# Performance work log

Hardware: AMD Instinct MI355X
Metric: run time of the kernel (lower is better)

The kernel has to match this reference:

```python
import jax, jax.numpy as jnp
import numpy as np

V = 6          # num_variables
K = 6          # codebook_size
D = 32         # embedding_dim
C = 3          # channels
B = 64         # batch
N = K ** V     # 46656 codebook combinations
EPS = 1e-5     # torch BatchNorm eps
ENTROPY_SCALE = 0.1


def setup_inputs() -> dict:
    key = jax.random.key(0)
    ks = jax.random.split(key, 40)
    i = iter(range(40))
    def rn(shape, s):
        return jax.random.normal(ks[next(i)], shape, dtype=jnp.float32) * s
    def rv(shape):
        return 0.5 + 0.5 * jax.random.uniform(ks[next(i)], shape, dtype=jnp.float32)
    inp = {
        'x': jax.random.normal(ks[next(i)], (B, C, 7, 7), dtype=jnp.float32),
        # encoder
        'conv_w': rn((256, C, 7, 7), 0.08), 'conv_b': rn((256,), 0.01),
        'ebn2_g': 1.0 + rn((256,), 0.1), 'ebn2_b': rn((256,), 0.1),
        'fc1_w': rn((1024, 256), 0.06), 'fc1_b': rn((1024,), 0.01),
        'ebn1_g': 1.0 + rn((1024,), 0.1), 'ebn1_b': rn((1024,), 0.1),
        'fc2_w': rn((V * K, 1024), 0.03), 'fc2_b': rn((V * K,), 0.01),
        # quantizer embeddings (V separate codebooks)
        'embeds': jax.random.normal(ks[next(i)], (V, K, D), dtype=jnp.float32),
        # decoder
        'dfc1_w': rn((1024, V * D), 0.07), 'dfc1_b': rn((1024,), 0.01),
        'dbn1_g': 1.0 + rn((1024,), 0.1), 'dbn1_b': rn((1024,), 0.1),
        'dbn1_rm': rn((1024,), 0.1), 'dbn1_rv': rv((1024,)),
        'dfc2_w': rn((256, 1024), 0.03), 'dfc2_b': rn((256,), 0.01),
        'dbn2_g': 1.0 + rn((256,), 0.1), 'dbn2_b': rn((256,), 0.1),
        'dbn2_rm': rn((256,), 0.1), 'dbn2_rv': rv((256,)),
        'dct1_w': rn((256, 16, 7, 7), 0.05), 'dct1_b': rn((16,), 0.01),
        'dbn3_g': 1.0 + rn((16,), 0.1), 'dbn3_b': rn((16,), 0.1),
        'dbn3_rm': rn((16,), 0.1), 'dbn3_rv': rv((16,)),
        'dct2_w': rn((16, C), 0.2), 'dct2_b': rn((C,), 0.01),
    }
    return inp


def _bn_eval(t, g, b, rm, rvar):
    # eval-mode BatchNorm (running stats); params broadcast over leading dims
    return g * (t - rm) * jax.lax.rsqrt(rvar + EPS) + b


def _bn_train(t, g, b):
    # train-mode BatchNorm1d on (B, F): biased batch statistics over dim 0
    m = t.mean(0)
    v = ((t - m) ** 2).mean(0)
    return g * (t - m) * jax.lax.rsqrt(v + EPS) + b


def _decode_all(embeds, dfc1_w, dfc1_b, dbn1_g, dbn1_b, dbn1_rm, dbn1_rv,
                dfc2_w, dfc2_b, dbn2_g, dbn2_b, dbn2_rm, dbn2_rv,
                dct1_w, dct1_b, dbn3_g, dbn3_b, dbn3_rm, dbn3_rv,
                dct2_w, dct2_b):
    # enumerate all K^V index tuples in itertools.product order (first var slowest)
    idx = jnp.arange(N)
    powers = K ** (V - 1 - jnp.arange(V))
    combos = (idx[:, None] // powers[None, :]) % K          # (N, V)
    z = embeds[jnp.arange(V)[None, :], combos]              # (N, V, D) gather
    h = z.reshape(N, V * D) @ dfc1_w.T + dfc1_b             # (N, 1024)
    h = jax.nn.relu(_bn_eval(h, dbn1_g, dbn1_b, dbn1_rm, dbn1_rv))
    h = h @ dfc2_w.T + dfc2_b                               # (N, 256)
    h = jax.nn.relu(_bn_eval(h, dbn2_g, dbn2_b, dbn2_rm, dbn2_rv))
    # ConvTranspose2d(256,16,7,stride=2) on 1x1 input == einsum with full kernel
    h = jnp.einsum('ni,iohw->nohw', h, dct1_w) + dct1_b[:, None, None]  # (N,16,7,7)
    h = jax.nn.relu(_bn_eval(h, dbn3_g[:, None, None], dbn3_b[:, None, None],
                             dbn3_rm[:, None, None], dbn3_rv[:, None, None]))
    # ConvTranspose2d(16,C,1,1) == pointwise channel mix
    em = jnp.einsum('nihw,io->nohw', h, dct2_w) + dct2_b[:, None, None]  # (N,C,7,7)
    return em


def reference(x, conv_w, conv_b, ebn2_g, ebn2_b, fc1_w, fc1_b, ebn1_g, ebn1_b,
              fc2_w, fc2_b, embeds, dfc1_w, dfc1_b, dbn1_g, dbn1_b, dbn1_rm,
              dbn1_rv, dfc2_w, dfc2_b, dbn2_g, dbn2_b, dbn2_rm, dbn2_rv,
              dct1_w, dct1_b, dbn3_g, dbn3_b, dbn3_rm, dbn3_rv, dct2_w, dct2_b):
    # emission means for every codebook combination (batched decode, BN eval)
    em = _decode_all(embeds, dfc1_w, dfc1_b, dbn1_g, dbn1_b, dbn1_rm, dbn1_rv,
                     dfc2_w, dfc2_b, dbn2_g, dbn2_b, dbn2_rm, dbn2_rv,
                     dct1_w, dct1_b, dbn3_g, dbn3_b, dbn3_rm, dbn3_rv,
                     dct2_w, dct2_b)                         # (N, C, 7, 7)
    # encoder: Conv2d(C,256,7) on 7x7 input collapses to a single GEMM
    e = jnp.einsum('bchw,ochw->bo', x, conv_w) + conv_b      # (B, 256)
    e = jax.nn.relu(_bn_train(e, ebn2_g, ebn2_b))
    e = e @ fc1_w.T + fc1_b                                  # (B, 1024)
    e = jax.nn.relu(_bn_train(e, ebn1_g, ebn1_b))
    logits = e @ fc2_w.T + fc2_b                             # (B, V*K)
    # quantizer
    latent_dist = jax.nn.softmax(logits.reshape(B, V, K), axis=-1)
    latent_loss = ENTROPY_SCALE * jnp.sum(
        latent_dist * jnp.log(latent_dist + 1e-10), axis=(1, 2))
    # obs logits: -0.5 * ||em - x||^2 summed over (C,H,W), via expanded form
    E = em.reshape(N, -1)                                    # (N, 147)
    X = x.reshape(B, -1)                                     # (B, 147)
    obs = -0.5 * (jnp.sum(E * E, -1)[None, :]
                  - 2.0 * (X @ E.T)
                  + jnp.sum(X * X, -1)[:, None])             # (B, N)
    obs_logits = obs.reshape((B,) + (K,) * V)
    return obs_logits, latent_dist, latent_loss
```

## Files before the change

### kernel.cpp

```cpp
#include <hip/hip_runtime.h>
#include <math.h>

#define EPSF 1e-5f
#define NNC 46656

typedef __attribute__((ext_vector_type(4))) float  f32x4;
typedef __attribute__((ext_vector_type(8))) short  short8;
typedef __attribute__((ext_vector_type(8))) unsigned short ushort8;
typedef __attribute__((ext_vector_type(4))) unsigned int uint4v;

__device__ __forceinline__ float bf2f(unsigned short u) {
    unsigned int x = ((unsigned int)u) << 16;
    return __builtin_bit_cast(float, x);
}
__device__ __forceinline__ unsigned short f2bf(float f) {
    unsigned int x = __builtin_bit_cast(unsigned int, f);
    unsigned int r = (x + 0x7fffu + ((x >> 16) & 1u)) >> 16;
    return (unsigned short)r;
}

__device__ __forceinline__ short8 packrelu8(ushort8 H8, ushort8 S8) {
    uint4v H = __builtin_bit_cast(uint4v, H8);
    uint4v S = __builtin_bit_cast(uint4v, S8);
    uint4v O;
#pragma unroll
    for (int d = 0; d < 4; ++d) {
        float hlo = __builtin_bit_cast(float, H[d] << 16);
        float hhi = __builtin_bit_cast(float, H[d] & 0xffff0000u);
        float slo = __builtin_bit_cast(float, S[d] << 16);
        float shi = __builtin_bit_cast(float, S[d] & 0xffff0000u);
        unsigned int rlo = __builtin_bit_cast(unsigned int, fmaxf(hlo + slo, 0.f));
        unsigned int rhi = __builtin_bit_cast(unsigned int, fmaxf(hhi + shi, 0.f));
        O[d] = __builtin_amdgcn_perm(rhi, rlo, 0x07060302u);
    }
    return __builtin_bit_cast(short8, O);
}

#define WS_SH    37888u
#define WS_S3    148480u
#define WS_W2BF  259072u
#define WS_C2    390144u
#define WS_W3BF  390400u
#define WS_C3    490752u
#define WS_XBF   490768u
#define WS_SX2   495888u
#define WS_E1T   495952u
#define WS_E2T   512336u
#define WS_FLAG  577872u

#define OBS_SIZE (64*NNC)
#define DIST_OFF OBS_SIZE
#define LOSS_OFF (OBS_SIZE + 64*36)

#define LDS_BYTES 53248


__global__ void dvae_k1(const float* __restrict__ x,
                        const float* __restrict__ conv_w, const float* __restrict__ conv_b,
                        const float* __restrict__ ebn2_g, const float* __restrict__ ebn2_b,
                        const float* __restrict__ embeds, const float* __restrict__ dfc1_w,
                        const float* __restrict__ dfc1_b,
                        const float* __restrict__ dbn1_g, const float* __restrict__ dbn1_b,
                        const float* __restrict__ dbn1_rm, const float* __restrict__ dbn1_rv,
                        const float* __restrict__ dfc2_w, const float* __restrict__ dfc2_b,
                        const float* __restrict__ dbn2_g, const float* __restrict__ dbn2_b,
                        const float* __restrict__ dbn2_rm, const float* __restrict__ dbn2_rv,
                        const float* __restrict__ dct1_w, const float* __restrict__ dct1_b,
                        const float* __restrict__ dbn3_g, const float* __restrict__ dbn3_b,
                        const float* __restrict__ dbn3_rm, const float* __restrict__ dbn3_rv,
                        float* __restrict__ ws) {
    __shared__ float sbuf[12544];
    int bx = blockIdx.x, tid = threadIdx.x;
    if (bx < 64) {
        float* wtile = sbuf;
        float* semb  = sbuf + 3088;
        float* Pt    = sbuf + 4240;
        float* c1s   = sbuf + 4960;
        int j0 = bx * 16;
        for (int e = tid; e < 16 * 192; e += 256)
            wtile[(e / 192) * 193 + (e % 192)] = dfc1_w[j0 * 192 + e];
        for (int e = tid; e < 1152; e += 256) semb[e] = embeds[e];
        __syncthreads();
        for (int e = tid; e < 576; e += 256) {
            int vk = e >> 4, jL = e & 15;
            int v = vk / 6;
            int j = j0 + jL;
            const float* wrow = &wtile[jL * 193 + v * 32];
            const float* ep = &semb[vk * 32];
            float dot = 0.f;
#pragma unroll
            for (int d = 0; d < 32; ++d) dot += wrow[d] * ep[d];
            float s1 = dbn1_g[j] * rsqrtf(dbn1_rv[j] + EPSF);
            Pt[vk * 20 + jL] = s1 * dot;
        }
        if (tid < 16) {
            int j = j0 + tid;
            float s = dbn1_g[j] * rsqrtf(dbn1_rv[j] + EPSF);
            c1s[tid] = s * dfc1_b[j] + dbn1_b[j] - dbn1_rm[j] * s;
        }
        __syncthreads();
        unsigned short* Sh = (unsigned short*)(ws + WS_SH);
        unsigned short* S3 = (unsigned short*)(ws + WS_S3);
        for (int e = tid; e < 216 * 16; e += 256) {
            int gh = e >> 4, jL = e & 15;
            int d0 = gh / 36, d1 = (gh / 6) % 6, d2 = gh % 6;
            float vh = c1s[jL] + Pt[d0 * 20 + jL] + Pt[(6 + d1) * 20 + jL] + Pt[(12 + d2) * 20 + jL];
            float vs = Pt[(18 + d0) * 20 + jL] + Pt[(24 + d1) * 20 + jL] + Pt[(30 + d2) * 20 + jL];
            Sh[gh * 1024 + j0 + jL] = f2bf(vh);
            S3[gh * 1024 + j0 + jL] = f2bf(vs);
        }
    } else if (bx < 320) {
        int t = (bx - 64) * 256 + tid;
        int i = t >> 8, kq = (t & 255) * 4;
        float s2 = dbn2_g[i] * rsqrtf(dbn2_rv[i] + EPSF);
        float4 w = *(const float4*)(dfc2_w + i * 1024 + kq);
        unsigned short* dst = (unsigned short*)(ws + WS_W2BF) + i * 1024 + kq;
        dst[0] = f2bf(s2 * w.x); dst[1] = f2bf(s2 * w.y);
        dst[2] = f2bf(s2 * w.z); dst[3] = f2bf(s2 * w.w);
        if (kq == 0) ws[WS_C2 + i] = s2 * dfc2_b[i] + dbn2_b[i] - dbn2_rm[i] * s2;
    } else if (bx < 336) {
        int blk = bx - 320;
        for (int e = tid; e < 12544; e += 256) sbuf[e] = dct1_w[blk * 12544 + e];
        __syncthreads();
        unsigned short* W3 = (unsigned short*)(ws + WS_W3BF);
        for (int e = tid; e < 1568; e += 256) {
            int up = e >> 1, k8 = (e & 1) * 8;
            int o = up & 15, hw = up >> 4;
            float s3 = dbn3_g[o] * rsqrtf(dbn3_rv[o] + EPSF);
            ushort8 ov;
#pragma unroll
            for (int t2 = 0; t2 < 8; ++t2)
                ov[t2] = f2bf(s3 * sbuf[(k8 + t2) * 784 + o * 49 + hw]);
            *(ushort8*)(W3 + up * 256 + blk * 16 + k8) = ov;
        }
        if (blk == 0 && tid < 16) {
            float s = dbn3_g[tid] * rsqrtf(dbn3_rv[tid] + EPSF);
            ws[WS_C3 + tid] = s * dct1_b[tid] + dbn3_b[tid] - dbn3_rm[tid] * s;
        }
    } else if (bx == 336) {
        unsigned short* Xb = (unsigned short*)(ws + WS_XBF);
        if (tid == 0) *(int*)(ws + WS_FLAG) = 0;
        if (tid < 64) {
            const float* xp = x + tid * 147;
            float s = 0.f;
            for (int qq = 0; qq < 147; ++qq) { float v = xp[qq]; s += v * v; }
            ws[WS_SX2 + tid] = s;
        }
        for (int e = tid; e < 64 * 160; e += 256) {
            int b = e / 160, col = e % 160;
            float v = 0.f;
            if (col < 147) { int hw = col / 3, c = col % 3; v = x[b * 147 + c * 49 + hw]; }
            Xb[e] = f2bf(v);
        }
    } else {
        int blk = bx - 337;
        for (int e = tid; e < 9408; e += 256) sbuf[e] = x[e];
        __syncthreads();
        int b = tid & 63;
        int oL = __builtin_amdgcn_readfirstlane(tid >> 6);
        int o = blk * 4 + oL;
        const float* wp = conv_w + o * 147;
        float acc = conv_b[o];
#pragma unroll 7
        for (int qq = 0; qq < 147; ++qq) acc += sbuf[b * 147 + qq] * wp[qq];
        float m = acc;
#pragma unroll
        for (int s = 1; s < 64; s <<= 1) m += __shfl_xor(m, s);
        m *= (1.f / 64.f);
        float d = acc - m;
        float var = d * d;
#pragma unroll
        for (int s = 1; s < 64; s <<= 1) var += __shfl_xor(var, s);
        var *= (1.f / 64.f);
        float y = ebn2_g[o] * d * rsqrtf(var + EPSF) + ebn2_b[o];
        ws[WS_E1T + o * 64 + b] = fmaxf(y, 0.f);
    }
}


__launch_bounds__(256, 3)
__global__ void dvae_k3(const unsigned short* __restrict__ Sh,
                        const unsigned short* __restrict__ S3g,
                        const unsigned short* __restrict__ W2,
                        const float* __restrict__ c2g,
                        const unsigned short* __restrict__ W3,
                        const float* __restrict__ c3g,
                        const float* __restrict__ d2wg,
                        const float* __restrict__ d2bg,
                        const unsigned short* __restrict__ Xg,
                        const float* __restrict__ sx2g,
                        const float* __restrict__ fc1_w, const float* __restrict__ fc1_b,
                        const float* __restrict__ ebn1_g, const float* __restrict__ ebn1_b,
                        const float* __restrict__ e1T,
                        float* __restrict__ e2T,
                        int* __restrict__ flag,
                        const float* __restrict__ fc2_w,
                        const float* __restrict__ fc2_b,
                        float* __restrict__ out) {
    extern __shared__ char sm[];
    int tid = threadIdx.x;

    if (blockIdx.x < 256) {
        int blk = blockIdx.x;
        int b = tid & 63;
        int jL = __builtin_amdgcn_readfirstlane(tid >> 6);
        int j = blk * 4 + jL;
        const float* wp = fc1_w + j * 256;
        float acc = fc1_b[j];
#pragma unroll 8
        for (int o = 0; o < 256; ++o) acc += e1T[o * 64 + b] * wp[o];
        float m = acc;
#pragma unroll
        for (int s = 1; s < 64; s <<= 1) m += __shfl_xor(m, s);
        m *= (1.f / 64.f);
        float d = acc - m;
        float var = d * d;
#pragma unroll
        for (int s = 1; s < 64; s <<= 1) var += __shfl_xor(var, s);
        var *= (1.f / 64.f);
        float y = ebn1_g[j] * d * rsqrtf(var + EPSF) + ebn1_b[j];
        e2T[j * 64 + b] = fmaxf(y, 0.f);
        __syncthreads();
        if (tid == 0) { __threadfence(); atomicAdd(flag, 1); }
        return;
    }

    if (blockIdx.x == 256) {
        if (tid == 0) {
            while (atomicAdd(flag, 0) < 256) __builtin_amdgcn_s_sleep(8);
        }
        __syncthreads();
        float* wch = (float*)sm;
        float* ech = (float*)(sm + 18432);
        float* LG  = (float*)sm;
        int b = tid & 63;
        int wvU = __builtin_amdgcn_readfirstlane(tid >> 6);
        float accv[9];
#pragma unroll
        for (int it = 0; it < 9; ++it) accv[it] = 0.f;
        for (int ch = 0; ch < 8; ++ch) {
            __syncthreads();
            for (int e = tid; e < 36 * 128; e += 256)
                wch[e] = fc2_w[(e >> 7) * 1024 + ch * 128 + (e & 127)];
            for (int e = tid; e < 128 * 64; e += 256)
                ech[e] = e2T[(ch * 128 + (e >> 6)) * 64 + (e & 63)];
            __syncthreads();
            for (int jl = 0; jl < 128; ++jl) {
                float ev = ech[jl * 64 + b];
#pragma unroll
                for (int it = 0; it < 9; ++it)
                    accv[it] += ev * wch[(wvU + it * 4) * 128 + jl];
            }
        }
        __syncthreads();
#pragma unroll
        for (int it = 0; it < 9; ++it) {
            int o = wvU + it * 4;
            LG[b * 36 + o] = accv[it] + fc2_b[o];
        }
        __syncthreads();
        if (tid < 64) {
            float loss = 0.f;
#pragma unroll
            for (int v = 0; v < 6; ++v) {
                float mx = -1e30f;
#pragma unroll
                for (int k = 0; k < 6; ++k) mx = fmaxf(mx, LG[tid * 36 + v * 6 + k]);
                float s = 0.f, ex[6];
#pragma unroll
                for (int k = 0; k < 6; ++k) { ex[k] = expf(LG[tid * 36 + v * 6 + k] - mx); s += ex[k]; }
                float inv = 1.f / s;
#pragma unroll
                for (int k = 0; k < 6; ++k) {
                    float dd = ex[k] * inv;
                    out[DIST_OFF + tid * 36 + v * 6 + k] = dd;
                    loss += dd * logf(dd + 1e-10f);
                }
            }
            out[LOSS_OFF + tid] = 0.1f * loss;
        }
        return;
    }

    int wv = tid >> 6, lane = tid & 63, l15 = lane & 15, q = lane >> 4;
    int db = blockIdx.x - 257;
    int g0 = (db / 27) * 8, r0 = (db % 27) * 8;
    unsigned short* emL = (unsigned short*)sm;
    unsigned short* h2L = (unsigned short*)(sm + 20480);
    float* sE2p = (float*)(sm + 20480);
    float* sE2f = (float*)(sm + 21504);
    char* Ast = sm;

    f32x4 acc[4][4];
#pragma unroll
    for (int a = 0; a < 4; ++a)
#pragma unroll
        for (int b = 0; b < 4; ++b) acc[a][b] = (f32x4){0.f, 0.f, 0.f, 0.f};

    int gh_t = g0 + (lane >> 3);
    int r_t  = r0 + (lane & 7);
    const unsigned short* shp = Sh  + gh_t * 1024 + wv * 32;
    const unsigned short* s3p = S3g + r_t  * 1024 + wv * 32;
    const unsigned short* bbase = W2 + (wv * 64 + l15) * 1024 + q * 8;
    int Xw = (lane & 7) << 4;
    int Xr = (l15 & 7) << 4;

    ushort8 rsh[4], rs3[4];
#pragma unroll
    for (int i = 0; i < 4; ++i) {
        rsh[i] = *(const ushort8*)(shp + i * 8);
        rs3[i] = *(const ushort8*)(s3p + i * 8);
    }
    short8 bpre[4];
#pragma unroll
    for (int j = 0; j < 4; ++j) bpre[j] = *(const short8*)(bbase + j * 16384);
#pragma unroll
    for (int i = 0; i < 4; ++i)
        *(short8*)(Ast + lane * 256 + ((wv * 64 + i * 16) ^ Xw)) = packrelu8(rsh[i], rs3[i]);
    __syncthreads();

    for (int c = 0; c < 8; ++c) {
        int cb = (c & 1) << 14;
        if (c < 7) {
            const unsigned short* p1 = shp + (c + 1) * 128;
            const unsigned short* p3 = s3p + (c + 1) * 128;
#pragma unroll
            for (int i = 0; i < 4; ++i) {
                rsh[i] = *(const ushort8*)(p1 + i * 8);
                rs3[i] = *(const ushort8*)(p3 + i * 8);
            }
        }
#pragma unroll
        for (int ss = 0; ss < 4; ++ss) {
            int s = c * 4 + ss;
            short8 af[4];
#pragma unroll
            for (int mt = 0; mt < 4; ++mt)
                af[mt] = *(const short8*)(Ast + cb + (mt * 16 + l15) * 256 + ((ss * 64 + q * 16) ^ Xr));
            short8 bcur[4];
#pragma unroll
            for (int j = 0; j < 4; ++j) bcur[j] = bpre[j];
            if (s < 31) {
#pragma unroll
                for (int j = 0; j < 4; ++j) bpre[j] = *(const short8*)(bbase + j * 16384 + (s + 1) * 32);
            }
#pragma unroll
            for (int mt = 0; mt < 4; ++mt)
#pragma unroll
                for (int j = 0; j < 4; ++j)
                    acc[mt][j] = __builtin_amdgcn_mfma_f32_16x16x32_bf16(af[mt], bcur[j], acc[mt][j], 0, 0, 0);
        }
        if (c < 7) {
            int nb = ((c + 1) & 1) << 14;
#pragma unroll
            for (int i = 0; i < 4; ++i)
                *(short8*)(Ast + nb + lane * 256 + ((wv * 64 + i * 16) ^ Xw)) = packrelu8(rsh[i], rs3[i]);
        }
        __syncthreads();
    }

#pragma unroll
    for (int j = 0; j < 4; ++j) {
        int i = wv * 64 + j * 16 + l15;
        float cc = c2g[i];
#pragma unroll
        for (int mt = 0; mt < 4; ++mt)
#pragma unroll
            for (int r = 0; r < 4; ++r) {
                int m = mt * 16 + q * 4 + r;
                h2L[((i >> 3) * 64 + m) * 8 + (i & 7)] = f2bf(fmaxf(acc[mt][j][r] + cc, 0.f));
            }
    }
    __syncthreads();

    float c3q[4], dwq0[4], dwq1[4], dwq2[4];
#pragma unroll
    for (int r = 0; r < 4; ++r) {
        int o = q * 4 + r;
        c3q[r]  = c3g[o];
        dwq0[r] = d2wg[o * 3 + 0];
        dwq1[r] = d2wg[o * 3 + 1];
        dwq2[r] = d2wg[o * 3 + 2];
    }
    float db0 = d2bg[0], db1 = d2bg[1], db2 = d2bg[2];
    float sE2acc[4] = {0.f, 0.f, 0.f, 0.f};

    for (int c = wv; c < 13; c += 4) {
        int hw0 = c * 4;
        f32x4 a2[4][4];
#pragma unroll
        for (int a = 0; a < 4; ++a)
#pragma unroll
            for (int b = 0; b < 4; ++b) a2[a][b] = (f32x4){0.f, 0.f, 0.f, 0.f};
        const unsigned short* b3[4];
#pragma unroll
        for (int j = 0; j < 4; ++j) {
            int hw = hw0 + j; if (hw > 48) hw = 48;
            b3[j] = W3 + (hw * 16 + l15) * 256 + q * 8;
        }
        short8 bpre2[4];
#pragma unroll
        for (int j = 0; j < 4; ++j) bpre2[j] = *(const short8*)(b3[j]);
#pragma unroll
        for (int s = 0; s < 8; ++s) {
            short8 bcur[4];
#pragma unroll
            for (int j = 0; j < 4; ++j) bcur[j] = bpre2[j];
            if (s < 7) {
#pragma unroll
                for (int j = 0; j < 4; ++j) bpre2[j] = *(const short8*)(b3[j] + (s + 1) * 32);
            }
            short8 af[4];
#pragma unroll
            for (int mt = 0; mt < 4; ++mt)
                af[mt] = *(const short8*)(h2L + ((s * 4 + q) * 64 + mt * 16 + l15) * 8);
#pragma unroll
            for (int mt = 0; mt < 4; ++mt)
#pragma unroll
                for (int j = 0; j < 4; ++j)
                    a2[mt][j] = __builtin_amdgcn_mfma_f32_16x16x32_bf16(bcur[j], af[mt], a2[mt][j], 0, 0, 0);
        }
#pragma unroll
        for (int j = 0; j < 4; ++j) {
            int hw = hw0 + j;
            if (hw <= 48) {
#pragma unroll
                for (int mt = 0; mt < 4; ++mt) {
                    float p0 = 0.f, p1 = 0.f, p2 = 0.f;
#pragma unroll
                    for (int r = 0; r < 4; ++r) {
                        float h = fmaxf(a2[mt][j][r] + c3q[r], 0.f);
                        p0 += h * dwq0[r]; p1 += h * dwq1[r]; p2 += h * dwq2[r];
                    }
                    p0 += __shfl_xor(p0, 16); p0 += __shfl_xor(p0, 32);
                    p1 += __shfl_xor(p1, 16); p1 += __shfl_xor(p1, 32);
                    p2 += __shfl_xor(p2, 16); p2 += __shfl_xor(p2, 32);
                    unsigned short u0 = f2bf(p0 + db0), u1 = f2bf(p1 + db1), u2 = f2bf(p2 + db2);
                    float f0 = bf2f(u0), f1 = bf2f(u1), f2v = bf2f(u2);
                    if (q == 0) {
                        sE2acc[mt] += f0 * f0 + f1 * f1 + f2v * f2v;
                        unsigned short* er = emL + (mt * 16 + l15) * 160 + hw * 3;
                        er[0] = u0; er[1] = u1; er[2] = u2;
                    }
                }
            }
        }
    }
    __syncthreads();
    if (q == 0) {
#pragma unroll
        for (int mt = 0; mt < 4; ++mt) sE2p[wv * 64 + mt * 16 + l15] = sE2acc[mt];
    }
    for (int e = tid; e < 64 * 13; e += 256) emL[(e / 13) * 160 + 147 + (e % 13)] = 0;
    __syncthreads();
    if (tid < 64) sE2f[tid] = sE2p[tid] + sE2p[64 + tid] + sE2p[128 + tid] + sE2p[192 + tid];
    __syncthreads();

    f32x4 aO[4];
#pragma unroll
    for (int j = 0; j < 4; ++j) aO[j] = (f32x4){0.f, 0.f, 0.f, 0.f};
    const unsigned short* xrow = Xg + (wv * 16 + l15) * 160 + q * 8;
#pragma unroll
    for (int s = 0; s < 5; ++s) {
        short8 af = *(const short8*)(xrow + s * 32);
#pragma unroll
        for (int j = 0; j < 4; ++j) {
            short8 bfv = *(const short8*)(emL + (j * 16 + l15) * 160 + s * 32 + q * 8);
            aO[j] = __builtin_amdgcn_mfma_f32_16x16x32_bf16(af, bfv, aO[j], 0, 0, 0);
        }
    }
    int b0 = wv * 16 + q * 4;
    float sxv[4];
#pragma unroll
    for (int r = 0; r < 4; ++r) sxv[r] = sx2g[b0 + r];
#pragma unroll
    for (int j = 0; j < 4; ++j) {
        int rloc = j * 16 + l15;
        int n = (g0 + (rloc >> 3)) * 216 + r0 + (rloc & 7);
        float he = 0.5f * sE2f[rloc];
#pragma unroll
        for (int r = 0; r < 4; ++r)
            out[(size_t)(b0 + r) * NNC + n] = aO[j][r] - he - 0.5f * sxv[r];
    }
}


extern "C" void kernel_launch(void* const* d_in, const int* in_sizes, int n_in,
                              void* d_out, int out_size, void* d_ws, size_t ws_size,
                              hipStream_t stream) {
    const float* x       = (const float*)d_in[0];
    const float* conv_w  = (const float*)d_in[1];
    const float* conv_b  = (const float*)d_in[2];
    const float* ebn2_g  = (const float*)d_in[3];
    const float* ebn2_b  = (const float*)d_in[4];
    const float* fc1_w   = (const float*)d_in[5];
    const float* fc1_b   = (const float*)d_in[6];
    const float* ebn1_g  = (const float*)d_in[7];
    const float* ebn1_b  = (const float*)d_in[8];
    const float* fc2_w   = (const float*)d_in[9];
    const float* fc2_b   = (const float*)d_in[10];
    const float* embeds  = (const float*)d_in[11];
    const float* dfc1_w  = (const float*)d_in[12];
    const float* dfc1_b  = (const float*)d_in[13];
    const float* dbn1_g  = (const float*)d_in[14];
    const float* dbn1_b  = (const float*)d_in[15];
    const float* dbn1_rm = (const float*)d_in[16];
    const float* dbn1_rv = (const float*)d_in[17];
    const float* dfc2_w  = (const float*)d_in[18];
    const float* dfc2_b  = (const float*)d_in[19];
    const float* dbn2_g  = (const float*)d_in[20];
    const float* dbn2_b  = (const float*)d_in[21];
    const float* dbn2_rm = (const float*)d_in[22];
    const float* dbn2_rv = (const float*)d_in[23];
    const float* dct1_w  = (const float*)d_in[24];
    const float* dct1_b  = (const float*)d_in[25];
    const float* dbn3_g  = (const float*)d_in[26];
    const float* dbn3_b  = (const float*)d_in[27];
    const float* dbn3_rm = (const float*)d_in[28];
    const float* dbn3_rv = (const float*)d_in[29];
    const float* dct2_w  = (const float*)d_in[30];
    const float* dct2_b  = (const float*)d_in[31];

    float* ws  = (float*)d_ws;
    float* out = (float*)d_out;

    dvae_k1<<<401, 256, 0, stream>>>(x, conv_w, conv_b, ebn2_g, ebn2_b,
                                     embeds, dfc1_w, dfc1_b, dbn1_g, dbn1_b, dbn1_rm, dbn1_rv,
                                     dfc2_w, dfc2_b, dbn2_g, dbn2_b, dbn2_rm, dbn2_rv,
                                     dct1_w, dct1_b, dbn3_g, dbn3_b, dbn3_rm, dbn3_rv, ws);

    hipFuncSetAttribute(reinterpret_cast<const void*>(dvae_k3),
                        hipFuncAttributeMaxDynamicSharedMemorySize, LDS_BYTES);
    dvae_k3<<<986, 256, LDS_BYTES, stream>>>(
        (const unsigned short*)(ws + WS_SH), (const unsigned short*)(ws + WS_S3),
        (const unsigned short*)(ws + WS_W2BF), ws + WS_C2,
        (const unsigned short*)(ws + WS_W3BF), ws + WS_C3,
        dct2_w, dct2_b,
        (const unsigned short*)(ws + WS_XBF), ws + WS_SX2,
        fc1_w, fc1_b, ebn1_g, ebn1_b,
        ws + WS_E1T, ws + WS_E2T, (int*)(ws + WS_FLAG),
        fc2_w, fc2_b, out);
}
```

Baseline: 259.1 us.

## Fuse prep and main kernels into one launch with atomic-flag dependencies

Merges the preprocessing kernel and the main decode/obs kernel into a single persistent-style launch. Producer blocks increment global counters and consumer blocks spin-wait on them, replacing the kernel boundary with fine-grained dependencies. This removes one launch and the full-grid barrier, letting the encoder chain overlap with decoder prep. It adds a memset for the flags and relies on low-index blocks being scheduled first, which risks deadlock or spin overhead if the ordering assumption fails.

```diff
diff --git a/kernel.cpp b/kernel.cpp
--- a/kernel.cpp
+++ b/kernel.cpp
@@ -54,23 +54,30 @@
 
 #define LDS_BYTES 53248
 
-
-__global__ void dvae_k1(const float* __restrict__ x,
-                        const float* __restrict__ conv_w, const float* __restrict__ conv_b,
-                        const float* __restrict__ ebn2_g, const float* __restrict__ ebn2_b,
-                        const float* __restrict__ embeds, const float* __restrict__ dfc1_w,
-                        const float* __restrict__ dfc1_b,
-                        const float* __restrict__ dbn1_g, const float* __restrict__ dbn1_b,
-                        const float* __restrict__ dbn1_rm, const float* __restrict__ dbn1_rv,
-                        const float* __restrict__ dfc2_w, const float* __restrict__ dfc2_b,
-                        const float* __restrict__ dbn2_g, const float* __restrict__ dbn2_b,
-                        const float* __restrict__ dbn2_rm, const float* __restrict__ dbn2_rv,
-                        const float* __restrict__ dct1_w, const float* __restrict__ dct1_b,
-                        const float* __restrict__ dbn3_g, const float* __restrict__ dbn3_b,
-                        const float* __restrict__ dbn3_rm, const float* __restrict__ dbn3_rv,
-                        float* __restrict__ ws) {
-    __shared__ float sbuf[12544];
+__launch_bounds__(256, 3)
+__global__ void dvae_all(const float* __restrict__ x,
+                         const float* __restrict__ conv_w, const float* __restrict__ conv_b,
+                         const float* __restrict__ ebn2_g, const float* __restrict__ ebn2_b,
+                         const float* __restrict__ embeds,
+                         const float* __restrict__ dfc1_w, const float* __restrict__ dfc1_b,
+                         const float* __restrict__ dbn1_g, const float* __restrict__ dbn1_b,
+                         const float* __restrict__ dbn1_rm, const float* __restrict__ dbn1_rv,
+                         const float* __restrict__ dfc2_w, const float* __restrict__ dfc2_b,
+                         const float* __restrict__ dbn2_g, const float* __restrict__ dbn2_b,
+                         const float* __restrict__ dbn2_rm, const float* __restrict__ dbn2_rv,
+                         const float* __restrict__ dct1_w, const float* __restrict__ dct1_b,
+                         const float* __restrict__ dbn3_g, const float* __restrict__ dbn3_b,
+                         const float* __restrict__ dbn3_rm, const float* __restrict__ dbn3_rv,
+                         const float* __restrict__ dct2_w, const float* __restrict__ dct2_b,
+                         const float* __restrict__ fc1_w, const float* __restrict__ fc1_b,
+                         const float* __restrict__ ebn1_g, const float* __restrict__ ebn1_b,
+                         const float* __restrict__ fc2_w, const float* __restrict__ fc2_b,
+                         float* ws, float* out) {
+    extern __shared__ char sm[];
+    float* sbuf = (float*)sm;
     int bx = blockIdx.x, tid = threadIdx.x;
+    int* flags = (int*)(ws + WS_FLAG);
+
     if (bx < 64) {
         float* wtile = sbuf;
         float* semb  = sbuf + 3088;
@@ -109,7 +116,12 @@
             Sh[gh * 1024 + j0 + jL] = f2bf(vh);
             S3[gh * 1024 + j0 + jL] = f2bf(vs);
         }
-    } else if (bx < 320) {
+        __syncthreads();
+        if (tid == 0) { __threadfence(); atomicAdd(&flags[0], 1); }
+        return;
+    }
+
+    if (bx < 320) {
         int t = (bx - 64) * 256 + tid;
         int i = t >> 8, kq = (t & 255) * 4;
         float s2 = dbn2_g[i] * rsqrtf(dbn2_rv[i] + EPSF);
@@ -118,7 +130,12 @@
         dst[0] = f2bf(s2 * w.x); dst[1] = f2bf(s2 * w.y);
         dst[2] = f2bf(s2 * w.z); dst[3] = f2bf(s2 * w.w);
         if (kq == 0) ws[WS_C2 + i] = s2 * dfc2_b[i] + dbn2_b[i] - dbn2_rm[i] * s2;
-    } else if (bx < 336) {
+        __syncthreads();
+        if (tid == 0) { __threadfence(); atomicAdd(&flags[0], 1); }
+        return;
+    }
+
+    if (bx < 336) {
         int blk = bx - 320;
         for (int e = tid; e < 12544; e += 256) sbuf[e] = dct1_w[blk * 12544 + e];
         __syncthreads();
@@ -137,9 +154,13 @@
             float s = dbn3_g[tid] * rsqrtf(dbn3_rv[tid] + EPSF);
             ws[WS_C3 + tid] = s * dct1_b[tid] + dbn3_b[tid] - dbn3_rm[tid] * s;
         }
-    } else if (bx == 336) {
+        __syncthreads();
+        if (tid == 0) { __threadfence(); atomicAdd(&flags[0], 1); }
+        return;
+    }
+
+    if (bx == 336) {
         unsigned short* Xb = (unsigned short*)(ws + WS_XBF);
-        if (tid == 0) *(int*)(ws + WS_FLAG) = 0;
         if (tid < 64) {
             const float* xp = x + tid * 147;
             float s = 0.f;
@@ -152,7 +173,12 @@
             if (col < 147) { int hw = col / 3, c = col % 3; v = x[b * 147 + c * 49 + hw]; }
             Xb[e] = f2bf(v);
         }
-    } else {
+        __syncthreads();
+        if (tid == 0) { __threadfence(); atomicAdd(&flags[0], 1); }
+        return;
+    }
+
+    if (bx < 401) {
         int blk = bx - 337;
         for (int e = tid; e < 9408; e += 256) sbuf[e] = x[e];
         __syncthreads();
@@ -174,34 +200,19 @@
         var *= (1.f / 64.f);
         float y = ebn2_g[o] * d * rsqrtf(var + EPSF) + ebn2_b[o];
         ws[WS_E1T + o * 64 + b] = fmaxf(y, 0.f);
-    }
-}
-
-
-__launch_bounds__(256, 3)
-__global__ void dvae_k3(const unsigned short* __restrict__ Sh,
-                        const unsigned short* __restrict__ S3g,
-                        const unsigned short* __restrict__ W2,
-                        const float* __restrict__ c2g,
-                        const unsigned short* __restrict__ W3,
-                        const float* __restrict__ c3g,
-                        const float* __restrict__ d2wg,
-                        const float* __restrict__ d2bg,
-                        const unsigned short* __restrict__ Xg,
-                        const float* __restrict__ sx2g,
-                        const float* __restrict__ fc1_w, const float* __restrict__ fc1_b,
-                        const float* __restrict__ ebn1_g, const float* __restrict__ ebn1_b,
-                        const float* __restrict__ e1T,
-                        float* __restrict__ e2T,
-                        int* __restrict__ flag,
-                        const float* __restrict__ fc2_w,
-                        const float* __restrict__ fc2_b,
-                        float* __restrict__ out) {
-    extern __shared__ char sm[];
-    int tid = threadIdx.x;
-
-    if (blockIdx.x < 256) {
-        int blk = blockIdx.x;
+        __syncthreads();
+        if (tid == 0) { __threadfence(); atomicAdd(&flags[1], 1); }
+        return;
+    }
+
+    if (bx < 657) {
+        if (tid == 0) {
+            while (atomicAdd(&flags[1], 0) < 64) __builtin_amdgcn_s_sleep(8);
+        }
+        __syncthreads();
+        const float* e1T = ws + WS_E1T;
+        float* e2T = ws + WS_E2T;
+        int blk = bx - 401;
         int b = tid & 63;
         int jL = __builtin_amdgcn_readfirstlane(tid >> 6);
         int j = blk * 4 + jL;
@@ -221,15 +232,16 @@
         float y = ebn1_g[j] * d * rsqrtf(var + EPSF) + ebn1_b[j];
         e2T[j * 64 + b] = fmaxf(y, 0.f);
         __syncthreads();
-        if (tid == 0) { __threadfence(); atomicAdd(flag, 1); }
-        return;
-    }
-
-    if (blockIdx.x == 256) {
+        if (tid == 0) { __threadfence(); atomicAdd(&flags[2], 1); }
+        return;
+    }
+
+    if (bx == 657) {
         if (tid == 0) {
-            while (atomicAdd(flag, 0) < 256) __builtin_amdgcn_s_sleep(8);
-        }
-        __syncthreads();
+            while (atomicAdd(&flags[2], 0) < 256) __builtin_amdgcn_s_sleep(8);
+        }
+        __syncthreads();
+        const float* e2T = ws + WS_E2T;
         float* wch = (float*)sm;
         float* ech = (float*)(sm + 18432);
         float* LG  = (float*)sm;
@@ -282,8 +294,22 @@
         return;
     }
 
+    if (tid == 0) {
+        while (atomicAdd(&flags[0], 0) < 337) __builtin_amdgcn_s_sleep(8);
+    }
+    __syncthreads();
+
+    const unsigned short* Sh  = (const unsigned short*)(ws + WS_SH);
+    const unsigned short* S3g = (const unsigned short*)(ws + WS_S3);
+    const unsigned short* W2  = (const unsigned short*)(ws + WS_W2BF);
+    const float* c2g = ws + WS_C2;
+    const unsigned short* W3  = (const unsigned short*)(ws + WS_W3BF);
+    const float* c3g = ws + WS_C3;
+    const unsigned short* Xg  = (const unsigned short*)(ws + WS_XBF);
+    const float* sx2g = ws + WS_SX2;
+
     int wv = tid >> 6, lane = tid & 63, l15 = lane & 15, q = lane >> 4;
-    int db = blockIdx.x - 257;
+    int db = bx - 658;
     int g0 = (db / 27) * 8, r0 = (db % 27) * 8;
     unsigned short* emL = (unsigned short*)sm;
     unsigned short* h2L = (unsigned short*)(sm + 20480);
@@ -378,11 +404,11 @@
     for (int r = 0; r < 4; ++r) {
         int o = q * 4 + r;
         c3q[r]  = c3g[o];
-        dwq0[r] = d2wg[o * 3 + 0];
-        dwq1[r] = d2wg[o * 3 + 1];
-        dwq2[r] = d2wg[o * 3 + 2];
-    }
-    float db0 = d2bg[0], db1 = d2bg[1], db2 = d2bg[2];
+        dwq0[r] = dct2_w[o * 3 + 0];
+        dwq1[r] = dct2_w[o * 3 + 1];
+        dwq2[r] = dct2_w[o * 3 + 2];
+    }
+    float db0 = dct2_b[0], db1 = dct2_b[1], db2 = dct2_b[2];
     float sE2acc[4] = {0.f, 0.f, 0.f, 0.f};
 
     for (int c = wv; c < 13; c += 4) {
@@ -524,20 +550,15 @@
     float* ws  = (float*)d_ws;
     float* out = (float*)d_out;
 
-    dvae_k1<<<401, 256, 0, stream>>>(x, conv_w, conv_b, ebn2_g, ebn2_b,
-                                     embeds, dfc1_w, dfc1_b, dbn1_g, dbn1_b, dbn1_rm, dbn1_rv,
-                                     dfc2_w, dfc2_b, dbn2_g, dbn2_b, dbn2_rm, dbn2_rv,
-                                     dct1_w, dct1_b, dbn3_g, dbn3_b, dbn3_rm, dbn3_rv, ws);
-
-    hipFuncSetAttribute(reinterpret_cast<const void*>(dvae_k3),
+    hipMemsetAsync((void*)(ws + WS_FLAG), 0, 16, stream);
+
+    hipFuncSetAttribute(reinterpret_cast<const void*>(dvae_all),
                         hipFuncAttributeMaxDynamicSharedMemorySize, LDS_BYTES);
-    dvae_k3<<<986, 256, LDS_BYTES, stream>>>(
-        (const unsigned short*)(ws + WS_SH), (const unsigned short*)(ws + WS_S3),
-        (const unsigned short*)(ws + WS_W2BF), ws + WS_C2,
-        (const unsigned short*)(ws + WS_W3BF), ws + WS_C3,
-        dct2_w, dct2_b,
-        (const unsigned short*)(ws + WS_XBF), ws + WS_SX2,
-        fc1_w, fc1_b, ebn1_g, ebn1_b,
-        ws + WS_E1T, ws + WS_E2T, (int*)(ws + WS_FLAG),
-        fc2_w, fc2_b, out);
+    dvae_all<<<1387, 256, LDS_BYTES, stream>>>(
+        x, conv_w, conv_b, ebn2_g, ebn2_b, embeds,
+        dfc1_w, dfc1_b, dbn1_g, dbn1_b, dbn1_rm, dbn1_rv,
+        dfc2_w, dfc2_b, dbn2_g, dbn2_b, dbn2_rm, dbn2_rv,
+        dct1_w, dct1_b, dbn3_g, dbn3_b, dbn3_rm, dbn3_rv,
+        dct2_w, dct2_b, fc1_w, fc1_b, ebn1_g, ebn1_b, fc2_w, fc2_b,
+        ws, out);
 }
```

After: 277.5 us. +7.1%, slower.
